# Kernel optimization log

Hardware: AMD Instinct MI355X
Metric: run time of the kernel (lower is better)

Reference implementation:

```python
import jax, jax.numpy as jnp
import numpy as np

NB = 32          # graph_batch_size
NEG_SLOPE = 0.2  # GATv2Conv leaky_relu slope


def _gat_spatial(X, V_Adap, Wl, bl, Wr, br, att, we, gat_bias, Wfc, bfc):
    # X: (B,T,N,F). GATv2 runs per time step on G diagonal blocks of size NB.
    B, T, N, F = X.shape
    G = N // NB
    Xb = X.reshape(B, T, G, NB, F)
    gl = jnp.einsum('btgnf,cf->btgnc', Xb, Wl) + bl  # lin_l (source msgs)
    gr = jnp.einsum('btgnf,cf->btgnc', Xb, Wr) + br  # lin_r (target)
    # diagonal blocks of the learned adjacency logits
    idx = jnp.arange(G)
    Vg = V_Adap[0].reshape(G, NB, G, NB)[idx, :, idx, :]   # (G, j_src, i_tgt)
    attr = jax.nn.sigmoid(Vg)                              # all > 0 => dense edges
    eye = jnp.eye(NB, dtype=bool)
    # PyG: remove self loops, then add self loops with fill_value='mean'
    off = jnp.where(eye, 0.0, attr)
    self_attr = off.sum(axis=1) / (NB - 1)                 # mean incoming per target
    attr_eff = jnp.where(eye, self_attr[:, None, :], attr) # (G, j, i)
    ef = attr_eff[..., None] * we                          # lin_edge, (G,j,i,C)
    ef = jnp.swapaxes(ef, 1, 2)                            # (G,i,j,C)
    # edges only cover flattened node ids 0..NB-1 => attention only for sample 0
    gl0, gr0 = gl[0], gr[0]                                # (T,G,NB,C)
    pre = gl0[:, :, None, :, :] + gr0[:, :, :, None, :] + ef[None]  # (T,G,i,j,C)
    S = jnp.einsum('tgijc,c->tgij', jax.nn.leaky_relu(pre, NEG_SLOPE), att)
    alpha = jax.nn.softmax(S, axis=-1)                     # softmax over sources j
    out0 = jnp.einsum('tgij,tgjc->tgic', alpha, gl0)
    # samples b>0: only the self loop -> alpha=1, message = gl
    out = jnp.concatenate([out0[None], gl[1:]], axis=0) + gat_bias
    y = jnp.einsum('btgnc,oc->btgno', out, Wfc) + bfc      # per-node fc
    return y.reshape(B, T, -1)                             # (B,T,N*spatial_out)


def _lstm_layer(x, Wih, Whh, bih, bhh):
    # torch LSTM gate order: i, f, g, o
    B, T, _ = x.shape
    H = Whh.shape[1]
    xg = jnp.einsum('bti,gi->btg', x, Wih) + bih           # (B,T,4H)
    xg = jnp.swapaxes(xg, 0, 1)                            # (T,B,4H)

    def step(carry, xt):
        h, c = carry
        g = xt + h @ Whh.T + bhh
        i, f, gg, o = jnp.split(g, 4, axis=-1)
        i = jax.nn.sigmoid(i)
        f = jax.nn.sigmoid(f)
        gg = jnp.tanh(gg)
        o = jax.nn.sigmoid(o)
        c = f * c + i * gg
        h = o * jnp.tanh(c)
        return (h, c), h

    h0 = jnp.zeros((B, H), x.dtype)
    _, hs = jax.lax.scan(step, (h0, h0), xg)
    return jnp.swapaxes(hs, 0, 1)                          # (B,T,H)


def setup_inputs() -> dict:
    key = jax.random.key(0)
    ks = jax.random.split(key, 24)
    B, T, N, F = 8, 64, 256, 64
    C, O, NC, H, HL = 128, 32, 16, 1024, 2
    s = 0.05
    inp = {
        'X': jax.random.normal(ks[0], (B, T, N, F), jnp.float32),
        'V_Adap': 0.2 + 0.05 * jax.random.normal(ks[1], (1, N, N), jnp.float32),
        'Wl': s * jax.random.normal(ks[2], (C, F), jnp.float32),
        'bl': s * jax.random.normal(ks[3], (C,), jnp.float32),
        'Wr': s * jax.random.normal(ks[4], (C, F), jnp.float32),
        'br': s * jax.random.normal(ks[5], (C,), jnp.float32),
        'att': s * jax.random.normal(ks[6], (C,), jnp.float32),
        'we': s * jax.random.normal(ks[7], (C,), jnp.float32),
        'gat_bias': s * jax.random.normal(ks[8], (C,), jnp.float32),
        'Wfc': s * jax.random.normal(ks[9], (O, C), jnp.float32),
        'bfc': s * jax.random.normal(ks[10], (O,), jnp.float32),
        'Wih0': s * jax.random.normal(ks[11], (4 * H, N * O), jnp.float32),
        'Whh0': s * jax.random.normal(ks[12], (4 * H, H), jnp.float32),
        'bih0': s * jax.random.normal(ks[13], (4 * H,), jnp.float32),
        'bhh0': s * jax.random.normal(ks[14], (4 * H,), jnp.float32),
        'Wih1': s * jax.random.normal(ks[15], (4 * H, H), jnp.float32),
        'Whh1': s * jax.random.normal(ks[16], (4 * H, H), jnp.float32),
        'bih1': s * jax.random.normal(ks[17], (4 * H,), jnp.float32),
        'bhh1': s * jax.random.normal(ks[18], (4 * H,), jnp.float32),
        'Wout': s * jax.random.normal(ks[19], (NC, H), jnp.float32),
        'bout': s * jax.random.normal(ks[20], (NC,), jnp.float32),
    }
    return inp


def reference(X, V_Adap, Wl, bl, Wr, br, att, we, gat_bias, Wfc, bfc,
              Wih0, Whh0, bih0, bhh0, Wih1, Whh1, bih1, bhh1, Wout, bout):
    s = _gat_spatial(X, V_Adap, Wl, bl, Wr, br, att, we, gat_bias, Wfc, bfc)
    h1 = _lstm_layer(s, Wih0, Whh0, bih0, bhh0)
    h2 = _lstm_layer(h1, Wih1, Whh1, bih1, bhh1)
    return h2[:, -1, :] @ Wout.T + bout                    # (B, num_classes)
```

## Files before the change

kernel.cpp:

```cpp
#include <hip/hip_runtime.h>
#include <cmath>

#define B_ 8
#define T_ 64
#define N_ 256
#define F_ 64
#define C_ 128
#define O_ 32
#define H_ 1024
#define NC_ 16

typedef __attribute__((ext_vector_type(8))) short bf16x8;
typedef __attribute__((ext_vector_type(4))) float f32x4;

__device__ __forceinline__ float sigf(float x){ return 1.f/(1.f+expf(-x)); }

__device__ __forceinline__ unsigned short f2bf(float f){
  unsigned int u = __float_as_uint(f);
  u += 0x7fff + ((u >> 16) & 1);
  return (unsigned short)(u >> 16);
}
__device__ __forceinline__ float bf2f(unsigned short s){
  return __uint_as_float(((unsigned int)s) << 16);
}

__device__ __forceinline__ void gload16(const void* g, void* l){
  __builtin_amdgcn_global_load_lds((const __attribute__((address_space(1))) void*)g,
                                   (__attribute__((address_space(3))) void*)l, 16, 0, 0);
}

__device__ __forceinline__ bf16x8 cvt8(const float* p){
  float4 a = *(const float4*)p, b = *(const float4*)(p + 4);
  bf16x8 r;
  r[0] = (short)f2bf(a.x); r[1] = (short)f2bf(a.y);
  r[2] = (short)f2bf(a.z); r[3] = (short)f2bf(a.w);
  r[4] = (short)f2bf(b.x); r[5] = (short)f2bf(b.y);
  r[6] = (short)f2bf(b.z); r[7] = (short)f2bf(b.w);
  return r;
}

#define TAGW(i) ((i) << 5)
#define NTAGW 8192

__global__ __launch_bounds__(256) void attr_kernel(const float* __restrict__ V, float* __restrict__ attr){
  __shared__ float sv[32][33];
  __shared__ float selfv[32];
  int g = blockIdx.x, tid = threadIdx.x;
  for (int idx = tid; idx < 1024; idx += 256){
    int j = idx >> 5, i = idx & 31;
    sv[j][i] = sigf(V[(size_t)(g*32 + j)*256 + g*32 + i]);
  }
  __syncthreads();
  if (tid < 32){
    float s = 0.f;
    for (int j = 0; j < 32; ++j) if (j != tid) s += sv[j][tid];
    selfv[tid] = s * (1.f/31.f);
  }
  __syncthreads();
  for (int idx = tid; idx < 1024; idx += 256){
    int j = idx >> 5, i = idx & 31;
    attr[g*1024 + idx] = (j == i) ? selfv[i] : sv[j][i];
  }
}

__global__ __launch_bounds__(256) void prep_kernel(
    const float* __restrict__ Wl, const float* __restrict__ Wr,
    const float* __restrict__ bl, const float* __restrict__ gb,
    const float* __restrict__ Wfc, const float* __restrict__ bfc,
    unsigned short* __restrict__ wcomb,
    float* __restrict__ bias_comb,
    unsigned short* __restrict__ wlr){
  __shared__ float wls[8192], wfcs[4096];
  int tid = threadIdx.x;
  for (int i = tid; i < 8192; i += 256) wls[i] = Wl[i];
  for (int i = tid; i < 4096; i += 256) wfcs[i] = Wfc[i];
  __syncthreads();
  for (int idx = tid; idx < 2048; idx += 256){
    int o = idx >> 6, f = idx & 63;
    float acc = 0.f;
    for (int c = 0; c < 128; ++c) acc = fmaf(wfcs[o*128 + c], wls[c*64 + f], acc);
    wcomb[idx] = f2bf(acc);
  }
  if (tid < 32){
    float acc = bfc[tid];
    for (int c = 0; c < 128; ++c) acc = fmaf(wfcs[tid*128 + c], bl[c] + gb[c], acc);
    bias_comb[tid] = acc;
  }
  for (int idx = tid; idx < 16384; idx += 256){
    int r = idx >> 6, f = idx & 63;
    wlr[idx] = f2bf(r < 128 ? wls[r*64 + f] : Wr[(r-128)*64 + f]);
  }
}

__global__ __launch_bounds__(256) void gemm_proj0(
    const float* __restrict__ X, const unsigned short* __restrict__ wlr,
    const float* __restrict__ bl, const float* __restrict__ br,
    float* __restrict__ gl0, float* __restrict__ gr0){
  int tid = threadIdx.x;
  int lane = tid & 63, w = tid >> 6;
  int lr = lane & 15, ko = lane >> 4;
  int row = blockIdx.x*64 + w*16 + lr;

  bf16x8 af[2];
  #pragma unroll
  for (int ks = 0; ks < 2; ++ks)
    af[ks] = cvt8(&X[(size_t)row*64 + ks*32 + ko*8]);

  f32x4 zero = {0.f,0.f,0.f,0.f};
  #pragma unroll 4
  for (int nt = 0; nt < 16; ++nt){
    f32x4 acc = zero;
    #pragma unroll
    for (int ks = 0; ks < 2; ++ks){
      bf16x8 bv = *(const bf16x8*)&wlr[(size_t)(nt*16 + lr)*64 + ks*32 + ko*8];
      acc = __builtin_amdgcn_mfma_f32_16x16x32_bf16(af[ks], bv, acc, 0, 0, 0);
    }
    int col = nt*16 + lr;
    #pragma unroll
    for (int v = 0; v < 4; ++v){
      int orow = blockIdx.x*64 + w*16 + ko*4 + v;
      if (col < 128) gl0[(size_t)orow*128 + col]        = acc[v] + bl[col];
      else           gr0[(size_t)orow*128 + (col-128)]  = acc[v] + br[col-128];
    }
  }
}

__global__ __launch_bounds__(256) void gemm_rest(
    const float* __restrict__ X, const unsigned short* __restrict__ wcomb,
    const float* __restrict__ bias_comb, unsigned short* __restrict__ xl){
  int tid = threadIdx.x;
  int lane = tid & 63, w = tid >> 6;
  int lr = lane & 15, ko = lane >> 4;
  int r0 = 16384 + blockIdx.x*256 + w*64;

  bf16x8 bv[2][2];
  #pragma unroll
  for (int nt = 0; nt < 2; ++nt)
    #pragma unroll
    for (int ks = 0; ks < 2; ++ks)
      bv[nt][ks] = *(const bf16x8*)&wcomb[(size_t)(nt*16 + lr)*64 + ks*32 + ko*8];

  f32x4 zero = {0.f,0.f,0.f,0.f};
  #pragma unroll
  for (int mt = 0; mt < 4; ++mt){
    int row = r0 + mt*16 + lr;
    bf16x8 af[2];
    #pragma unroll
    for (int ks = 0; ks < 2; ++ks)
      af[ks] = cvt8(&X[(size_t)row*64 + ks*32 + ko*8]);
    f32x4 acc0 = zero, acc1 = zero;
    #pragma unroll
    for (int ks = 0; ks < 2; ++ks){
      acc0 = __builtin_amdgcn_mfma_f32_16x16x32_bf16(af[ks], bv[0][ks], acc0, 0, 0, 0);
      acc1 = __builtin_amdgcn_mfma_f32_16x16x32_bf16(af[ks], bv[1][ks], acc1, 0, 0, 0);
    }
    #pragma unroll
    for (int v = 0; v < 4; ++v){
      int orow = r0 + mt*16 + ko*4 + v;
      xl[(size_t)orow*32 + lr]      = f2bf(acc0[v] + bias_comb[lr]);
      xl[(size_t)orow*32 + 16 + lr] = f2bf(acc1[v] + bias_comb[16 + lr]);
    }
  }
}

__global__ __launch_bounds__(256) void attn_kernel(
    const float* __restrict__ gl0, const float* __restrict__ gr0,
    const float* __restrict__ attr, const float* __restrict__ we, const float* __restrict__ att,
    const float* __restrict__ gbias, const float* __restrict__ Wfc, const float* __restrict__ bfc,
    unsigned short* __restrict__ xl){
  __shared__ float gls[32*129], grs[32*129], os_[32*129], Wfcs[32*129];
  __shared__ float ae[32*33], Ss[32*33];
  __shared__ float wes[128], atts[128];
  int tid = threadIdx.x, blk = blockIdx.x;
  int g = blk & 7, t = blk >> 3;

  const float* glp = gl0 + ((size_t)t*N_ + g*32)*C_;
  const float* grp = gr0 + ((size_t)t*N_ + g*32)*C_;
  for (int idx = tid; idx < 4096; idx += 256){
    int n = idx >> 7, c = idx & 127;
    gls[n*129 + c]  = glp[idx];
    grs[n*129 + c]  = grp[idx];
    Wfcs[n*129 + c] = Wfc[idx];
  }
  for (int idx = tid; idx < 1024; idx += 256) ae[(idx>>5)*33 + (idx&31)] = attr[g*1024 + idx];
  if (tid < 128){ wes[tid] = we[tid]; atts[tid] = att[tid]; }
  __syncthreads();

  int i = tid >> 3, jb = (tid & 7) * 4;
  float a0 = ae[(jb+0)*33 + i], a1 = ae[(jb+1)*33 + i], a2 = ae[(jb+2)*33 + i], a3 = ae[(jb+3)*33 + i];
  float s0 = 0.f, s1 = 0.f, s2 = 0.f, s3 = 0.f;
  for (int cc = 0; cc < 128; ++cc){
    float grv = grs[i*129 + cc];
    float wv = wes[cc], av = atts[cc];
    float p0 = gls[(jb+0)*129 + cc] + grv + a0*wv;
    float p1 = gls[(jb+1)*129 + cc] + grv + a1*wv;
    float p2 = gls[(jb+2)*129 + cc] + grv + a2*wv;
    float p3 = gls[(jb+3)*129 + cc] + grv + a3*wv;
    p0 = p0 > 0.f ? p0 : 0.2f*p0;
    p1 = p1 > 0.f ? p1 : 0.2f*p1;
    p2 = p2 > 0.f ? p2 : 0.2f*p2;
    p3 = p3 > 0.f ? p3 : 0.2f*p3;
    s0 = fmaf(p0, av, s0); s1 = fmaf(p1, av, s1);
    s2 = fmaf(p2, av, s2); s3 = fmaf(p3, av, s3);
  }
  Ss[i*33 + jb + 0] = s0; Ss[i*33 + jb + 1] = s1;
  Ss[i*33 + jb + 2] = s2; Ss[i*33 + jb + 3] = s3;
  __syncthreads();

  if (tid < 32){
    float mx = -1e30f;
    for (int j = 0; j < 32; ++j) mx = fmaxf(mx, Ss[tid*33 + j]);
    float sum = 0.f;
    for (int j = 0; j < 32; ++j) sum += expf(Ss[tid*33 + j] - mx);
    float inv = 1.f / sum;
    for (int j = 0; j < 32; ++j) Ss[tid*33 + j] = expf(Ss[tid*33 + j] - mx) * inv;
  }
  __syncthreads();

  int c2 = tid & 127, ibase = (tid >> 7) * 16;
  float gbv = gbias[c2];
  for (int p = 0; p < 16; ++p){
    int ii = ibase + p;
    float acc = 0.f;
    #pragma unroll
    for (int j = 0; j < 32; ++j) acc = fmaf(Ss[ii*33 + j], gls[j*129 + c2], acc);
    os_[ii*129 + c2] = acc + gbv;
  }
  __syncthreads();

  int o = tid & 31, n2b = tid >> 5;
  float bfv = bfc[o];
  for (int p = 0; p < 4; ++p){
    int n2 = n2b + 8*p;
    float acc = bfv;
    for (int cc = 0; cc < 128; ++cc)
      acc = fmaf(os_[n2*129 + cc], Wfcs[o*129 + cc], acc);
    xl[((size_t)t*N_ + g*32 + n2)*O_ + o] = f2bf(acc);
  }
}

__global__ __launch_bounds__(256) void f2b_kernel(const float* __restrict__ in,
                                                  unsigned short* __restrict__ out, int n4){
  int idx = blockIdx.x*256 + threadIdx.x;
  if (idx >= n4) return;
  float4 v = ((const float4*)in)[idx];
  ushort4 o;
  o.x = f2bf(v.x); o.y = f2bf(v.y); o.z = f2bf(v.z); o.w = f2bf(v.w);
  ((ushort4*)out)[idx] = o;
}

__global__ __launch_bounds__(256) void w2cat_kernel(const float* __restrict__ Whh1,
                                                    const float* __restrict__ Wih1,
                                                    unsigned short* __restrict__ w2){
  int row = blockIdx.x, tid = threadIdx.x;
  const float* a = Whh1 + (size_t)row*1024 + tid*4;
  const float* b = Wih1 + (size_t)row*1024 + tid*4;
  float4 va = *(const float4*)a, vb = *(const float4*)b;
  ushort4 oa, ob;
  oa.x = f2bf(va.x); oa.y = f2bf(va.y); oa.z = f2bf(va.z); oa.w = f2bf(va.w);
  ob.x = f2bf(vb.x); ob.y = f2bf(vb.y); ob.z = f2bf(vb.z); ob.w = f2bf(vb.w);
  *(ushort4*)&w2[(size_t)row*2048 + tid*4]        = oa;
  *(ushort4*)&w2[(size_t)row*2048 + 1024 + tid*4] = ob;
}

__global__ __launch_bounds__(256) void gemm_bf2s(
    const unsigned short* __restrict__ A, const unsigned short* __restrict__ W,
    float* __restrict__ Yp, int N, int K){
  __shared__ __align__(16) short As[2][64*64];
  __shared__ __align__(16) short Bs[2][128*64];
  int tid = threadIdx.x;
  int id = blockIdx.x;
  int ks = id >> 8, rest = id & 255;
  int xcd = rest & 7, local = rest >> 3;
  int nt = xcd*4 + (local & 3), mt = local >> 2;
  int m0 = mt*64, n0 = nt*128;
  int kbase = ks * (K >> 1);
  float* Y = Yp + (size_t)ks*512*N;
  int lane = tid & 63;
  int w = tid >> 6, wm = w >> 1, wn = w & 1;
  int lr = lane & 15, ko = lane >> 4;
  int wbase = tid & ~63;

  auto STAGE = [&](int buf, int kc){
    #pragma unroll
    for (int it = 0; it < 2; ++it){
      int chunk = it*256 + tid;
      int r = chunk >> 3, c8 = chunk & 7;
      int cs = (c8 ^ (r & 7)) << 3;
      gload16(&A[(size_t)(m0 + r)*K + kc + cs], &As[buf][(size_t)(it*256 + wbase)*8]);
    }
    #pragma unroll
    for (int it = 0; it < 4; ++it){
      int chunk = it*256 + tid;
      int r = chunk >> 3, c8 = chunk & 7;
      int cs = (c8 ^ (r & 7)) << 3;
      gload16(&W[(size_t)(n0 + r)*K + kc + cs], &Bs[buf][(size_t)(it*256 + wbase)*8]);
    }
  };

  f32x4 zero = {0.f,0.f,0.f,0.f};
  f32x4 acc[2][4] = {{zero,zero,zero,zero},{zero,zero,zero,zero}};

  STAGE(0, kbase);
  __syncthreads();
  int nk = K >> 7;
  for (int kt = 0; kt < nk; ++kt){
    int cur = kt & 1;
    if (kt + 1 < nk) STAGE(cur ^ 1, kbase + ((kt + 1) << 6));
    #pragma unroll
    for (int kk = 0; kk < 2; ++kk){
      int s = kk*4 + ko;
      bf16x8 af[2], bfv[4];
      #pragma unroll
      for (int m = 0; m < 2; ++m){
        int row = wm*32 + m*16 + lr;
        af[m] = *(const bf16x8*)&As[cur][row*64 + ((s ^ (row & 7)) << 3)];
      }
      #pragma unroll
      for (int n = 0; n < 4; ++n){
        int row = wn*64 + n*16 + lr;
        bfv[n] = *(const bf16x8*)&Bs[cur][row*64 + ((s ^ (row & 7)) << 3)];
      }
      #pragma unroll
      for (int m = 0; m < 2; ++m)
        #pragma unroll
        for (int n = 0; n < 4; ++n)
          acc[m][n] = __builtin_amdgcn_mfma_f32_16x16x32_bf16(af[m], bfv[n], acc[m][n], 0, 0, 0);
    }
    __syncthreads();
  }

  #pragma unroll
  for (int m = 0; m < 2; ++m)
    #pragma unroll
    for (int n = 0; n < 4; ++n)
      #pragma unroll
      for (int v = 0; v < 4; ++v){
        int row = m0 + wm*32 + m*16 + ko*4 + v;
        int col = n0 + wn*64 + n*16 + lr;
        Y[(size_t)row*N + col] = acc[m][n][v];
      }
}

__global__ __launch_bounds__(256) void ksum_kernel(
    const float* __restrict__ p0, const float* __restrict__ p1,
    const float* __restrict__ b1, const float* __restrict__ b2,
    float* __restrict__ Y, unsigned* __restrict__ syncw){
  int idx = blockIdx.x*256 + threadIdx.x;
  if (idx < NTAGW) syncw[idx] = 0u;
  int i4 = idx;
  float4 a = ((const float4*)p0)[i4];
  float4 b = ((const float4*)p1)[i4];
  int col = (i4 << 2) & 4095;
  float4 u = *(const float4*)&b1[col];
  float4 v = *(const float4*)&b2[col];
  float4 o;
  o.x = a.x + b.x + u.x + v.x;
  o.y = a.y + b.y + u.y + v.y;
  o.z = a.z + b.z + u.z + v.z;
  o.w = a.w + b.w + u.w + v.w;
  ((float4*)Y)[i4] = o;
}

__global__ __launch_bounds__(512) void lstm_persist(
    const unsigned short* __restrict__ whh0,
    const unsigned short* __restrict__ w2cat,
    const float* __restrict__ xg0,
    const float* __restrict__ bih1, const float* __restrict__ bhh1,
    unsigned short* __restrict__ h1seq,
    unsigned short* __restrict__ h2seq,
    unsigned* __restrict__ syncw){
  __shared__ float red[4][8][64];
  const int tid = threadIdx.x;
  const int lane = tid & 63, w = tid >> 6;
  const int g = w >> 2, ws = w & 3;
  const bool layer2 = (blockIdx.x >= 128);
  const int lb = layer2 ? (int)blockIdx.x - 128 : (int)blockIdx.x;
  const int lr = lane & 15, ko = lane >> 4;
  const int q = lr >> 2, dl = lr & 3;
  const int row = q*H_ + lb*8 + g*4 + dl;

  bf16x8 wreg[16];
  if (!layer2){
    const unsigned short* wrow = whh0 + (size_t)row*1024 + ws*256;
    #pragma unroll
    for (int kk = 0; kk < 8; ++kk) wreg[kk] = *(const bf16x8*)&wrow[kk*32 + ko*8];
  } else {
    const unsigned short* wrow = w2cat + (size_t)row*2048 + ws*512;
    #pragma unroll
    for (int kk = 0; kk < 16; ++kk) wreg[kk] = *(const bf16x8*)&wrow[kk*32 + ko*8];
  }

  const int g2 = tid >> 5, bt = (tid >> 2) & 7, dl2 = tid & 3;
  const int dimt = lb*8 + g2*4 + dl2;
  float creg = 0.f;
  float b2r[4] = {0.f,0.f,0.f,0.f};
  if (layer2 && tid < 64){
    #pragma unroll
    for (int qq = 0; qq < 4; ++qq) b2r[qq] = bih1[qq*H_ + dimt] + bhh1[qq*H_ + dimt];
  }
  const bf16x8 zero8 = {0,0,0,0,0,0,0,0};
  const int tt0 = layer2 ? 1 : 0;
  const int tt1 = layer2 ? 64 : 63;

  for (int tt = tt0; tt <= tt1; ++tt){
    const int tau = layer2 ? tt - 1 : tt;

    if (w == 0){
      const bool poll1 = layer2 || (tt > 0);
      if (poll1){
        const unsigned need1 = (unsigned)tt;
        const unsigned need2 = (unsigned)(tt - 1);
        unsigned* pa = syncw + TAGW(lane);
        unsigned* pb = syncw + TAGW(64 + lane);
        unsigned* pc = syncw + TAGW(128 + lane);
        unsigned* pd = syncw + TAGW(192 + lane);
        const bool poll2 = layer2 && (tt >= 2);
        for (;;){
          bool ok = (__hip_atomic_load(pa, __ATOMIC_RELAXED, __HIP_MEMORY_SCOPE_AGENT) >= need1)
                 && (__hip_atomic_load(pb, __ATOMIC_RELAXED, __HIP_MEMORY_SCOPE_AGENT) >= need1);
          if (poll2)
            ok = ok && (__hip_atomic_load(pc, __ATOMIC_RELAXED, __HIP_MEMORY_SCOPE_AGENT) >= need2)
                    && (__hip_atomic_load(pd, __ATOMIC_RELAXED, __HIP_MEMORY_SCOPE_AGENT) >= need2);
          if (__all(ok)) break;
          __builtin_amdgcn_s_sleep(1);
        }
      }
    }
    __syncthreads();

    f32x4 accv = {0.f,0.f,0.f,0.f};
    {
      const unsigned short* arow = nullptr;
      if (!layer2){
        if (tt > 0) arow = h1seq + ((size_t)(lr & 7)*T_ + (tt-1))*H_ + ws*256;
      } else {
        if (ws < 2){ if (tau > 0) arow = h2seq + ((size_t)(lr & 7)*T_ + (tau-1))*H_ + ws*512; }
        else         arow = h1seq + ((size_t)(lr & 7)*T_ + tau)*H_ + (ws-2)*512;
      }
      if (arow){
        f32x4 acc2 = {0.f,0.f,0.f,0.f};
        if (!layer2){
          #pragma unroll
          for (int kk = 0; kk < 8; ++kk){
            bf16x8 av = (lr < 8) ? *(const bf16x8*)&arow[kk*32 + ko*8] : zero8;
            if (kk & 1) acc2 = __builtin_amdgcn_mfma_f32_16x16x32_bf16(av, wreg[kk], acc2, 0, 0, 0);
            else        accv = __builtin_amdgcn_mfma_f32_16x16x32_bf16(av, wreg[kk], accv, 0, 0, 0);
          }
        } else {
          #pragma unroll
          for (int kk = 0; kk < 16; ++kk){
            bf16x8 av = (lr < 8) ? *(const bf16x8*)&arow[kk*32 + ko*8] : zero8;
            if (kk & 1) acc2 = __builtin_amdgcn_mfma_f32_16x16x32_bf16(av, wreg[kk], acc2, 0, 0, 0);
            else        accv = __builtin_amdgcn_mfma_f32_16x16x32_bf16(av, wreg[kk], accv, 0, 0, 0);
          }
        }
        accv = accv + acc2;
      }
    }
    #pragma unroll
    for (int v = 0; v < 4; ++v) red[v][w][lane] = accv[v];
    __syncthreads();

    if (w == 0){
      float pre[4];
      #pragma unroll
      for (int qq = 0; qq < 4; ++qq){
        int lsrc = (bt >> 2)*16 + qq*4 + dl2, v = bt & 3;
        pre[qq] = red[v][g2*4+0][lsrc] + red[v][g2*4+1][lsrc]
                + red[v][g2*4+2][lsrc] + red[v][g2*4+3][lsrc];
      }
      float pi, pf, pg, po;
      if (!layer2){
        size_t xb = ((size_t)bt*T_ + tt)*4096;
        pi = pre[0] + xg0[xb + 0*H_ + dimt];
        pf = pre[1] + xg0[xb + 1*H_ + dimt];
        pg = pre[2] + xg0[xb + 2*H_ + dimt];
        po = pre[3] + xg0[xb + 3*H_ + dimt];
      } else {
        pi = pre[0] + b2r[0]; pf = pre[1] + b2r[1];
        pg = pre[2] + b2r[2]; po = pre[3] + b2r[3];
      }
      float i_ = sigf(pi), f_ = sigf(pf), g_ = tanhf(pg), o_ = sigf(po);
      float cn = fmaf(f_, creg, i_*g_);
      creg = cn;
      float hn = o_ * tanhf(cn);
      unsigned short* hp = (layer2 ? h2seq : h1seq) + ((size_t)bt*T_ + tau)*H_ + dimt;
      __hip_atomic_store(hp, f2bf(hn), __ATOMIC_RELAXED, __HIP_MEMORY_SCOPE_AGENT);
      asm volatile("s_waitcnt vmcnt(0)" ::: "memory");
      if (lane == 0)
        __hip_atomic_store(syncw + TAGW((layer2 ? 128 : 0) + lb), (unsigned)(tau + 1),
                           __ATOMIC_RELAXED, __HIP_MEMORY_SCOPE_AGENT);
    }
  }
}

__global__ __launch_bounds__(128) void final_kernel(
    const unsigned short* __restrict__ h2_seq, const float* __restrict__ Wout,
    const float* __restrict__ bout, float* __restrict__ out){
  int tid = threadIdx.x;
  int b = tid >> 4, nc = tid & 15;
  const unsigned short* hp = h2_seq + ((size_t)b*T_ + (T_ - 1))*H_;
  const float* wp = Wout + nc*H_;
  float acc = bout[nc];
  for (int k = 0; k < 1024; ++k) acc = fmaf(bf2f(hp[k]), wp[k], acc);
  out[tid] = acc;
}

extern "C" void kernel_launch(void* const* d_in, const int* in_sizes, int n_in,
                              void* d_out, int out_size, void* d_ws, size_t ws_size,
                              hipStream_t stream){
  const float* X    = (const float*)d_in[0];
  const float* V    = (const float*)d_in[1];
  const float* Wl   = (const float*)d_in[2];
  const float* bl   = (const float*)d_in[3];
  const float* Wr   = (const float*)d_in[4];
  const float* br   = (const float*)d_in[5];
  const float* att  = (const float*)d_in[6];
  const float* we   = (const float*)d_in[7];
  const float* gb   = (const float*)d_in[8];
  const float* Wfc  = (const float*)d_in[9];
  const float* bfc  = (const float*)d_in[10];
  const float* Wih0 = (const float*)d_in[11];
  const float* Whh0 = (const float*)d_in[12];
  const float* bih0 = (const float*)d_in[13];
  const float* bhh0 = (const float*)d_in[14];
  const float* Wih1 = (const float*)d_in[15];
  const float* Whh1 = (const float*)d_in[16];
  const float* bih1 = (const float*)d_in[17];
  const float* bhh1 = (const float*)d_in[18];
  const float* Wout = (const float*)d_in[19];
  const float* bout = (const float*)d_in[20];

  float* ws   = (float*)d_ws;
  float* attr = ws;
  float* gl0  = attr + 8192;
  float* gr0  = gl0 + 2097152;
  float* xg0  = gr0 + 2097152;
  float* bias_comb = xg0 + 2097152;
  unsigned short* xl_bf  = (unsigned short*)(bias_comb + 64);
  unsigned short* w0_bf  = xl_bf + 4194304;
  unsigned short* wh0_bf = w0_bf + 33554432;
  unsigned short* w2_bf  = wh0_bf + 4194304;
  unsigned short* h1_bf  = w2_bf + 8388608;
  unsigned short* h2_bf  = h1_bf + 524288;
  unsigned short* wlr_bf = h2_bf + 524288;
  unsigned short* wcomb  = wlr_bf + 16384;
  unsigned* syncw = (unsigned*)xl_bf;
  (void)in_sizes; (void)n_in; (void)out_size; (void)ws_size;

  attr_kernel<<<8, 256, 0, stream>>>(V, attr);
  prep_kernel<<<1, 256, 0, stream>>>(Wl, Wr, bl, gb, Wfc, bfc, wcomb, bias_comb, wlr_bf);
  gemm_proj0<<<256, 256, 0, stream>>>(X, wlr_bf, bl, br, gl0, gr0);
  attn_kernel<<<512, 256, 0, stream>>>(gl0, gr0, attr, we, att, gb, Wfc, bfc, xl_bf);
  gemm_rest<<<448, 256, 0, stream>>>(X, wcomb, bias_comb, xl_bf);

  f2b_kernel<<<32768, 256, 0, stream>>>(Wih0, w0_bf, 8388608);
  f2b_kernel<<<4096, 256, 0, stream>>>(Whh0, wh0_bf, 1048576);
  w2cat_kernel<<<4096, 256, 0, stream>>>(Whh1, Wih1, w2_bf);

  gemm_bf2s<<<512, 256, 0, stream>>>(xl_bf, w0_bf, gl0, 4096, 8192);
  ksum_kernel<<<2048, 256, 0, stream>>>(gl0, gr0, bih0, bhh0, xg0, syncw);

  {
    void* args[] = {(void*)&wh0_bf, (void*)&w2_bf, (void*)&xg0,
                    (void*)&bih1, (void*)&bhh1, (void*)&h1_bf, (void*)&h2_bf,
                    (void*)&syncw};
    hipLaunchCooperativeKernel((const void*)lstm_persist, dim3(256), dim3(512),
                               args, 0, stream);
  }

  final_kernel<<<1, 128, 0, stream>>>(h2_bf, Wout, bout, (float*)d_out);
}
```

Baseline: 639.8 us.

## Shrink persistent LSTM to 24 blocks streaming repacked MFMA-ordered weights

```diff
diff --git a/kernel.cpp b/kernel.cpp
--- a/kernel.cpp
+++ b/kernel.cpp
@@ -40,7 +40,9 @@
 }
 
 #define TAGW(i) ((i) << 5)
-#define NTAGW 8192
+#define NTAGW 1024
+#define L1B 8
+#define L2B 16
 
 __global__ __launch_bounds__(256) void attr_kernel(const float* __restrict__ V, float* __restrict__ attr){
   __shared__ float sv[32][33];
@@ -249,18 +251,32 @@
   ((ushort4*)out)[idx] = o;
 }
 
-__global__ __launch_bounds__(256) void w2cat_kernel(const float* __restrict__ Whh1,
-                                                    const float* __restrict__ Wih1,
-                                                    unsigned short* __restrict__ w2){
-  int row = blockIdx.x, tid = threadIdx.x;
-  const float* a = Whh1 + (size_t)row*1024 + tid*4;
-  const float* b = Wih1 + (size_t)row*1024 + tid*4;
-  float4 va = *(const float4*)a, vb = *(const float4*)b;
-  ushort4 oa, ob;
-  oa.x = f2bf(va.x); oa.y = f2bf(va.y); oa.z = f2bf(va.z); oa.w = f2bf(va.w);
-  ob.x = f2bf(vb.x); ob.y = f2bf(vb.y); ob.z = f2bf(vb.z); ob.w = f2bf(vb.w);
-  *(ushort4*)&w2[(size_t)row*2048 + tid*4]        = oa;
-  *(ushort4*)&w2[(size_t)row*2048 + 1024 + tid*4] = ob;
+__global__ __launch_bounds__(256) void repack1_kernel(const float* __restrict__ Whh0,
+                                                      unsigned short* __restrict__ wp1){
+  int tot = blockIdx.x*256 + threadIdx.x;
+  int lane = tot & 63;
+  int q    = (tot >> 6) & 3;
+  int kt   = (tot >> 8) & 31;
+  int wv   = (tot >> 13) & 7;
+  int lb   = tot >> 16;
+  int row = q*1024 + lb*128 + wv*16 + (lane & 15);
+  int col = kt*32 + (lane >> 4)*8;
+  *(bf16x8*)&wp1[(size_t)tot*8] = cvt8(&Whh0[(size_t)row*1024 + col]);
+}
+
+__global__ __launch_bounds__(256) void repack2_kernel(const float* __restrict__ Whh1,
+                                                      const float* __restrict__ Wih1,
+                                                      unsigned short* __restrict__ wp2){
+  int tot = blockIdx.x*256 + threadIdx.x;
+  int lane = tot & 63;
+  int q    = (tot >> 6) & 3;
+  int kt   = (tot >> 8) & 31;
+  int wv   = (tot >> 13) & 7;
+  int lb2  = tot >> 16;
+  int row = q*1024 + lb2*64 + (wv & 3)*16 + (lane & 15);
+  int col = kt*32 + (lane >> 4)*8;
+  const float* src = (wv >> 2) ? Wih1 : Whh1;
+  *(bf16x8*)&wp2[(size_t)tot*8] = cvt8(&src[(size_t)row*1024 + col]);
 }
 
 __global__ __launch_bounds__(256) void gemm_bf2s(
@@ -363,135 +379,137 @@
 }
 
 __global__ __launch_bounds__(512) void lstm_persist(
-    const unsigned short* __restrict__ whh0,
-    const unsigned short* __restrict__ w2cat,
+    const unsigned short* __restrict__ wp1,
+    const unsigned short* __restrict__ wp2,
     const float* __restrict__ xg0,
     const float* __restrict__ bih1, const float* __restrict__ bhh1,
     unsigned short* __restrict__ h1seq,
     unsigned short* __restrict__ h2seq,
     unsigned* __restrict__ syncw){
-  __shared__ float red[4][8][64];
+  __shared__ float red[4][4][64][4];
   const int tid = threadIdx.x;
   const int lane = tid & 63, w = tid >> 6;
-  const int g = w >> 2, ws = w & 3;
-  const bool layer2 = (blockIdx.x >= 128);
-  const int lb = layer2 ? (int)blockIdx.x - 128 : (int)blockIdx.x;
+  const bool layer2 = (blockIdx.x >= L1B);
+  const int lb = layer2 ? (int)blockIdx.x - L1B : (int)blockIdx.x;
   const int lr = lane & 15, ko = lane >> 4;
-  const int q = lr >> 2, dl = lr & 3;
-  const int row = q*H_ + lb*8 + g*4 + dl;
-
-  bf16x8 wreg[16];
-  if (!layer2){
-    const unsigned short* wrow = whh0 + (size_t)row*1024 + ws*256;
-    #pragma unroll
-    for (int kk = 0; kk < 8; ++kk) wreg[kk] = *(const bf16x8*)&wrow[kk*32 + ko*8];
-  } else {
-    const unsigned short* wrow = w2cat + (size_t)row*2048 + ws*512;
-    #pragma unroll
-    for (int kk = 0; kk < 16; ++kk) wreg[kk] = *(const bf16x8*)&wrow[kk*32 + ko*8];
-  }
-
-  const int g2 = tid >> 5, bt = (tid >> 2) & 7, dl2 = tid & 3;
-  const int dimt = lb*8 + g2*4 + dl2;
-  float creg = 0.f;
+  const int wd = layer2 ? (w & 3) : w;
+  const int kc = layer2 ? (w >> 2) : 1;
+  const int dimw = layer2 ? (lb*64 + wd*16 + lr) : (lb*128 + wd*16 + lr);
+  const unsigned short* wpb = (layer2 ? wp2 : wp1) + (size_t)(lb*8 + w)*65536;
+
   float b2r[4] = {0.f,0.f,0.f,0.f};
-  if (layer2 && tid < 64){
-    #pragma unroll
-    for (int qq = 0; qq < 4; ++qq) b2r[qq] = bih1[qq*H_ + dimt] + bhh1[qq*H_ + dimt];
-  }
+  if (layer2 && w < 4){
+    #pragma unroll
+    for (int q = 0; q < 4; ++q) b2r[q] = bih1[q*H_ + dimw] + bhh1[q*H_ + dimw];
+  }
+  f32x4 creg = {0.f,0.f,0.f,0.f};
   const bf16x8 zero8 = {0,0,0,0,0,0,0,0};
-  const int tt0 = layer2 ? 1 : 0;
-  const int tt1 = layer2 ? 64 : 63;
+  const f32x4 zf = {0.f,0.f,0.f,0.f};
+  const int tt0 = layer2 ? 1 : 0, tt1 = layer2 ? 64 : 63;
 
   for (int tt = tt0; tt <= tt1; ++tt){
     const int tau = layer2 ? tt - 1 : tt;
 
-    if (w == 0){
-      const bool poll1 = layer2 || (tt > 0);
-      if (poll1){
-        const unsigned need1 = (unsigned)tt;
-        const unsigned need2 = (unsigned)(tt - 1);
-        unsigned* pa = syncw + TAGW(lane);
-        unsigned* pb = syncw + TAGW(64 + lane);
-        unsigned* pc = syncw + TAGW(128 + lane);
-        unsigned* pd = syncw + TAGW(192 + lane);
-        const bool poll2 = layer2 && (tt >= 2);
-        for (;;){
-          bool ok = (__hip_atomic_load(pa, __ATOMIC_RELAXED, __HIP_MEMORY_SCOPE_AGENT) >= need1)
-                 && (__hip_atomic_load(pb, __ATOMIC_RELAXED, __HIP_MEMORY_SCOPE_AGENT) >= need1);
-          if (poll2)
-            ok = ok && (__hip_atomic_load(pc, __ATOMIC_RELAXED, __HIP_MEMORY_SCOPE_AGENT) >= need2)
-                    && (__hip_atomic_load(pd, __ATOMIC_RELAXED, __HIP_MEMORY_SCOPE_AGENT) >= need2);
-          if (__all(ok)) break;
-          __builtin_amdgcn_s_sleep(1);
+    float xv[4][4];
+    if (!layer2 && ko < 2){
+      #pragma unroll
+      for (int q = 0; q < 4; ++q)
+        #pragma unroll
+        for (int v = 0; v < 4; ++v)
+          xv[q][v] = xg0[((size_t)(ko*4 + v)*T_ + tt)*4096 + q*H_ + dimw];
+    }
+
+    if (w == 0 && (layer2 || tt > 0)){
+      const unsigned* p = nullptr; unsigned need = 0;
+      if (!layer2){
+        if (lane < L1B){ p = syncw + TAGW(lane); need = (unsigned)tt; }
+      } else {
+        if (lane < L1B){ p = syncw + TAGW(lane); need = (unsigned)tt; }
+        else if (lane < L1B + L2B && tt >= 2){ p = syncw + TAGW(lane); need = (unsigned)(tt - 1); }
+      }
+      for (;;){
+        bool ok = true;
+        if (p) ok = (__hip_atomic_load(p, __ATOMIC_RELAXED, __HIP_MEMORY_SCOPE_AGENT) >= need);
+        if (__all(ok)) break;
+        __builtin_amdgcn_s_sleep(1);
+      }
+    }
+    __syncthreads();
+
+    f32x4 acc0 = zf, acc1 = zf, acc2 = zf, acc3 = zf;
+    const unsigned short* asrc = nullptr;
+    if (!layer2){
+      if (tt > 0) asrc = h1seq + ((size_t)(lr & 7)*T_ + (tt-1))*H_;
+    } else if (kc == 0){
+      if (tau > 0) asrc = h2seq + ((size_t)(lr & 7)*T_ + (tau-1))*H_;
+    } else {
+      asrc = h1seq + ((size_t)(lr & 7)*T_ + tau)*H_;
+    }
+    if (asrc){
+      #pragma unroll 8
+      for (int kt = 0; kt < 32; ++kt){
+        bf16x8 av = (lr < 8) ? *(const bf16x8*)&asrc[kt*32 + ko*8] : zero8;
+        const unsigned short* bb = wpb + kt*2048 + lane*8;
+        acc0 = __builtin_amdgcn_mfma_f32_16x16x32_bf16(av, *(const bf16x8*)&bb[0],    acc0, 0, 0, 0);
+        acc1 = __builtin_amdgcn_mfma_f32_16x16x32_bf16(av, *(const bf16x8*)&bb[512],  acc1, 0, 0, 0);
+        acc2 = __builtin_amdgcn_mfma_f32_16x16x32_bf16(av, *(const bf16x8*)&bb[1024], acc2, 0, 0, 0);
+        acc3 = __builtin_amdgcn_mfma_f32_16x16x32_bf16(av, *(const bf16x8*)&bb[1536], acc3, 0, 0, 0);
+      }
+    }
+
+    bool gate_lane;
+    float pre0[4], pre1[4], pre2[4], pre3[4];
+    if (!layer2){
+      gate_lane = (ko < 2);
+      if (gate_lane){
+        #pragma unroll
+        for (int v = 0; v < 4; ++v){
+          pre0[v] = acc0[v] + xv[0][v];
+          pre1[v] = acc1[v] + xv[1][v];
+          pre2[v] = acc2[v] + xv[2][v];
+          pre3[v] = acc3[v] + xv[3][v];
         }
       }
+    } else {
+      if (w >= 4){
+        #pragma unroll
+        for (int v = 0; v < 4; ++v){
+          red[0][wd][lane][v] = acc0[v];
+          red[1][wd][lane][v] = acc1[v];
+          red[2][wd][lane][v] = acc2[v];
+          red[3][wd][lane][v] = acc3[v];
+        }
+      }
+      __syncthreads();
+      gate_lane = (w < 4) && (ko < 2);
+      if (gate_lane){
+        #pragma unroll
+        for (int v = 0; v < 4; ++v){
+          pre0[v] = acc0[v] + red[0][wd][lane][v] + b2r[0];
+          pre1[v] = acc1[v] + red[1][wd][lane][v] + b2r[1];
+          pre2[v] = acc2[v] + red[2][wd][lane][v] + b2r[2];
+          pre3[v] = acc3[v] + red[3][wd][lane][v] + b2r[3];
+        }
+      }
+    }
+
+    if (gate_lane){
+      unsigned short* hdst = (layer2 ? h2seq : h1seq);
+      #pragma unroll
+      for (int v = 0; v < 4; ++v){
+        float i_ = sigf(pre0[v]), f_ = sigf(pre1[v]);
+        float g_ = tanhf(pre2[v]), o_ = sigf(pre3[v]);
+        float cn = fmaf(f_, creg[v], i_*g_);
+        creg[v] = cn;
+        float hn = o_ * tanhf(cn);
+        __hip_atomic_store(&hdst[((size_t)(ko*4 + v)*T_ + tau)*H_ + dimw], f2bf(hn),
+                           __ATOMIC_RELAXED, __HIP_MEMORY_SCOPE_AGENT);
+      }
     }
     __syncthreads();
-
-    f32x4 accv = {0.f,0.f,0.f,0.f};
-    {
-      const unsigned short* arow = nullptr;
-      if (!layer2){
-        if (tt > 0) arow = h1seq + ((size_t)(lr & 7)*T_ + (tt-1))*H_ + ws*256;
-      } else {
-        if (ws < 2){ if (tau > 0) arow = h2seq + ((size_t)(lr & 7)*T_ + (tau-1))*H_ + ws*512; }
-        else         arow = h1seq + ((size_t)(lr & 7)*T_ + tau)*H_ + (ws-2)*512;
-      }
-      if (arow){
-        f32x4 acc2 = {0.f,0.f,0.f,0.f};
-        if (!layer2){
-          #pragma unroll
-          for (int kk = 0; kk < 8; ++kk){
-            bf16x8 av = (lr < 8) ? *(const bf16x8*)&arow[kk*32 + ko*8] : zero8;
-            if (kk & 1) acc2 = __builtin_amdgcn_mfma_f32_16x16x32_bf16(av, wreg[kk], acc2, 0, 0, 0);
-            else        accv = __builtin_amdgcn_mfma_f32_16x16x32_bf16(av, wreg[kk], accv, 0, 0, 0);
-          }
-        } else {
-          #pragma unroll
-          for (int kk = 0; kk < 16; ++kk){
-            bf16x8 av = (lr < 8) ? *(const bf16x8*)&arow[kk*32 + ko*8] : zero8;
-            if (kk & 1) acc2 = __builtin_amdgcn_mfma_f32_16x16x32_bf16(av, wreg[kk], acc2, 0, 0, 0);
-            else        accv = __builtin_amdgcn_mfma_f32_16x16x32_bf16(av, wreg[kk], accv, 0, 0, 0);
-          }
-        }
-        accv = accv + acc2;
-      }
-    }
-    #pragma unroll
-    for (int v = 0; v < 4; ++v) red[v][w][lane] = accv[v];
-    __syncthreads();
-
-    if (w == 0){
-      float pre[4];
-      #pragma unroll
-      for (int qq = 0; qq < 4; ++qq){
-        int lsrc = (bt >> 2)*16 + qq*4 + dl2, v = bt & 3;
-        pre[qq] = red[v][g2*4+0][lsrc] + red[v][g2*4+1][lsrc]
-                + red[v][g2*4+2][lsrc] + red[v][g2*4+3][lsrc];
-      }
-      float pi, pf, pg, po;
-      if (!layer2){
-        size_t xb = ((size_t)bt*T_ + tt)*4096;
-        pi = pre[0] + xg0[xb + 0*H_ + dimt];
-        pf = pre[1] + xg0[xb + 1*H_ + dimt];
-        pg = pre[2] + xg0[xb + 2*H_ + dimt];
-        po = pre[3] + xg0[xb + 3*H_ + dimt];
-      } else {
-        pi = pre[0] + b2r[0]; pf = pre[1] + b2r[1];
-        pg = pre[2] + b2r[2]; po = pre[3] + b2r[3];
-      }
-      float i_ = sigf(pi), f_ = sigf(pf), g_ = tanhf(pg), o_ = sigf(po);
-      float cn = fmaf(f_, creg, i_*g_);
-      creg = cn;
-      float hn = o_ * tanhf(cn);
-      unsigned short* hp = (layer2 ? h2seq : h1seq) + ((size_t)bt*T_ + tau)*H_ + dimt;
-      __hip_atomic_store(hp, f2bf(hn), __ATOMIC_RELAXED, __HIP_MEMORY_SCOPE_AGENT);
-      asm volatile("s_waitcnt vmcnt(0)" ::: "memory");
-      if (lane == 0)
-        __hip_atomic_store(syncw + TAGW((layer2 ? 128 : 0) + lb), (unsigned)(tau + 1),
-                           __ATOMIC_RELAXED, __HIP_MEMORY_SCOPE_AGENT);
-    }
+    if (tid == 0)
+      __hip_atomic_store(syncw + TAGW(layer2 ? (L1B + lb) : lb), (unsigned)(tau + 1),
+                         __ATOMIC_RELAXED, __HIP_MEMORY_SCOPE_AGENT);
   }
 }
 
@@ -540,9 +558,9 @@
   float* bias_comb = xg0 + 2097152;
   unsigned short* xl_bf  = (unsigned short*)(bias_comb + 64);
   unsigned short* w0_bf  = xl_bf + 4194304;
-  unsigned short* wh0_bf = w0_bf + 33554432;
-  unsigned short* w2_bf  = wh0_bf + 4194304;
-  unsigned short* h1_bf  = w2_bf + 8388608;
+  unsigned short* wp1    = w0_bf + 33554432;
+  unsigned short* wp2    = wp1 + 4194304;
+  unsigned short* h1_bf  = wp2 + 8388608;
   unsigned short* h2_bf  = h1_bf + 524288;
   unsigned short* wlr_bf = h2_bf + 524288;
   unsigned short* wcomb  = wlr_bf + 16384;
@@ -556,17 +574,17 @@
   gemm_rest<<<448, 256, 0, stream>>>(X, wcomb, bias_comb, xl_bf);
 
   f2b_kernel<<<32768, 256, 0, stream>>>(Wih0, w0_bf, 8388608);
-  f2b_kernel<<<4096, 256, 0, stream>>>(Whh0, wh0_bf, 1048576);
-  w2cat_kernel<<<4096, 256, 0, stream>>>(Whh1, Wih1, w2_bf);
+  repack1_kernel<<<2048, 256, 0, stream>>>(Whh0, wp1);
+  repack2_kernel<<<4096, 256, 0, stream>>>(Whh1, Wih1, wp2);
 
   gemm_bf2s<<<512, 256, 0, stream>>>(xl_bf, w0_bf, gl0, 4096, 8192);
   ksum_kernel<<<2048, 256, 0, stream>>>(gl0, gr0, bih0, bhh0, xg0, syncw);
 
   {
-    void* args[] = {(void*)&wh0_bf, (void*)&w2_bf, (void*)&xg0,
+    void* args[] = {(void*)&wp1, (void*)&wp2, (void*)&xg0,
                     (void*)&bih1, (void*)&bhh1, (void*)&h1_bf, (void*)&h2_bf,
                     (void*)&syncw};
-    hipLaunchCooperativeKernel((const void*)lstm_persist, dim3(256), dim3(512),
+    hipLaunchCooperativeKernel((const void*)lstm_persist, dim3(L1B + L2B), dim3(512),
                                args, 0, stream);
   }
 
```

New measurement: 1.373 ms. 115% more time.
